# Kernel tuning notes

Measured on AMD Instinct MI355X. Metric: run time of the kernel, lower is better.

## Reference

```python
import jax, jax.numpy as jnp
import numpy as np

D_MODEL = 2048
NUM_EXPERTS = 64
TOP_K = 2
ALPHA = 0.01


def setup_inputs() -> dict:
    key = jax.random.key(0)
    kx, kw = jax.random.split(key)
    x = jax.random.normal(kx, (4, 4096, D_MODEL), dtype=jnp.float32)
    # kaiming-uniform-ish gate weight, bound = 1/sqrt(d_model)
    bound = 1.0 / np.sqrt(D_MODEL)
    W = jax.random.uniform(kw, (NUM_EXPERTS, D_MODEL), dtype=jnp.float32,
                           minval=-bound, maxval=bound)
    return {"x": x, "W": W}


def reference(x, W):
    bsz, seq, h = x.shape
    xf = x.reshape(-1, h)                       # [N, h], N = bsz*seq
    logits = xf @ W.T                            # [N, E]
    scores = jax.nn.softmax(logits, axis=-1)     # [N, E]
    topk_weight, topk_idx = jax.lax.top_k(scores, TOP_K)  # [N, k], [N, k]
    if TOP_K > 1:
        topk_weight = topk_weight / (topk_weight.sum(axis=-1, keepdims=True) + 1e-9)
    # aux loss (training path, alpha > 0)
    one_hot = jax.nn.one_hot(topk_idx.reshape(-1), NUM_EXPERTS, dtype=jnp.float32)
    freq = one_hot.mean(axis=0)                  # [E]
    Pi = scores.mean(axis=0)                     # [E]
    fi = freq * NUM_EXPERTS
    aux_loss = (Pi * fi).sum() * ALPHA
    return topk_weight, topk_idx, aux_loss
```

## Files before the change

### kernel.cpp

```cpp
#include <hip/hip_runtime.h>
#include <math.h>


#define D_MODEL     2048
#define NUM_EXPERTS 64
#define N_ROWS      16384
#define ALPHA       0.01f

#define BR      32
#define BK      32
#define THREADS 256

#define SX 36
#define SW 68
#define SL 72

__global__ __launch_bounds__(THREADS)
void router_fused(const float* __restrict__ x, const float* __restrict__ W,
                  float* __restrict__ out_w, float* __restrict__ out_i,
                  float* __restrict__ g_pi, float* __restrict__ g_cnt) {
    __shared__ float lx[BR * SX];
    __shared__ float lw[BK * SW];
    __shared__ float ll[BR * SL];
    __shared__ float apx[4][NUM_EXPERTS];
    __shared__ float acn[4][NUM_EXPERTS];

    const int tid = threadIdx.x;
    const int rb  = blockIdx.x * BR;

    const int srow = tid >> 3;
    const int skb  = (tid & 7) * 4;

    const float* xg  = x + (size_t)(rb + srow) * D_MODEL + skb;
    const float* wg0 = W + (size_t)srow        * D_MODEL + skb;
    const float* wg1 = W + (size_t)(srow + 32) * D_MODEL + skb;

    const int tx = tid & 15;
    const int ty = tid >> 4;
    const int r0 = ty * 2, r1 = ty * 2 + 1;
    const int eb = tx * 4;

    float acc[2][4] = {{0.f,0.f,0.f,0.f},{0.f,0.f,0.f,0.f}};

    float4 px  = *(const float4*)(xg);
    float4 pw0 = *(const float4*)(wg0);
    float4 pw1 = *(const float4*)(wg1);

    for (int kc = 0; kc < D_MODEL / BK; ++kc) {
        __syncthreads();
        *(float4*)&lx[srow * SX + skb] = px;
        lw[(skb + 0) * SW + srow] = pw0.x;
        lw[(skb + 1) * SW + srow] = pw0.y;
        lw[(skb + 2) * SW + srow] = pw0.z;
        lw[(skb + 3) * SW + srow] = pw0.w;
        lw[(skb + 0) * SW + srow + 32] = pw1.x;
        lw[(skb + 1) * SW + srow + 32] = pw1.y;
        lw[(skb + 2) * SW + srow + 32] = pw1.z;
        lw[(skb + 3) * SW + srow + 32] = pw1.w;
        if (kc + 1 < D_MODEL / BK) {
            const int o = (kc + 1) * BK;
            px  = *(const float4*)(xg  + o);
            pw0 = *(const float4*)(wg0 + o);
            pw1 = *(const float4*)(wg1 + o);
        }
        __syncthreads();

        #pragma unroll
        for (int kk = 0; kk < BK / 4; ++kk) {
            const float4 xa = *(const float4*)&lx[r0 * SX + kk * 4];
            const float4 xb = *(const float4*)&lx[r1 * SX + kk * 4];
            const float4 w0 = *(const float4*)&lw[(kk * 4 + 0) * SW + eb];
            const float4 w1 = *(const float4*)&lw[(kk * 4 + 1) * SW + eb];
            const float4 w2 = *(const float4*)&lw[(kk * 4 + 2) * SW + eb];
            const float4 w3 = *(const float4*)&lw[(kk * 4 + 3) * SW + eb];

            acc[0][0] += xa.x*w0.x + xa.y*w1.x + xa.z*w2.x + xa.w*w3.x;
            acc[0][1] += xa.x*w0.y + xa.y*w1.y + xa.z*w2.y + xa.w*w3.y;
            acc[0][2] += xa.x*w0.z + xa.y*w1.z + xa.z*w2.z + xa.w*w3.z;
            acc[0][3] += xa.x*w0.w + xa.y*w1.w + xa.z*w2.w + xa.w*w3.w;

            acc[1][0] += xb.x*w0.x + xb.y*w1.x + xb.z*w2.x + xb.w*w3.x;
            acc[1][1] += xb.x*w0.y + xb.y*w1.y + xb.z*w2.y + xb.w*w3.y;
            acc[1][2] += xb.x*w0.z + xb.y*w1.z + xb.z*w2.z + xb.w*w3.z;
            acc[1][3] += xb.x*w0.w + xb.y*w1.w + xb.z*w2.w + xb.w*w3.w;
        }
    }

    *(float4*)&ll[r0 * SL + eb] = make_float4(acc[0][0], acc[0][1], acc[0][2], acc[0][3]);
    *(float4*)&ll[r1 * SL + eb] = make_float4(acc[1][0], acc[1][1], acc[1][2], acc[1][3]);
    __syncthreads();

    const int wv   = tid >> 6;
    const int lane = tid & 63;
    float pi_acc  = 0.f;
    float cnt_acc = 0.f;

    for (int r8 = 0; r8 < 8; ++r8) {
        const int row = wv * 8 + r8;
        const float lg = ll[row * SL + lane];

        float m = lg;
        #pragma unroll
        for (int off = 32; off; off >>= 1) m = fmaxf(m, __shfl_xor(m, off));
        const float e = expf(lg - m);
        float s = e;
        #pragma unroll
        for (int off = 32; off; off >>= 1) s += __shfl_xor(s, off);
        const float score = e / s;

        float v1 = score; int i1 = lane;
        #pragma unroll
        for (int off = 32; off; off >>= 1) {
            const float ov = __shfl_xor(v1, off);
            const int   oi = __shfl_xor(i1, off);
            if (ov > v1 || (ov == v1 && oi < i1)) { v1 = ov; i1 = oi; }
        }
        float v2 = (lane == i1) ? -1.f : score; int i2 = lane;
        #pragma unroll
        for (int off = 32; off; off >>= 1) {
            const float ov = __shfl_xor(v2, off);
            const int   oi = __shfl_xor(i2, off);
            if (ov > v2 || (ov == v2 && oi < i2)) { v2 = ov; i2 = oi; }
        }

        if (lane == 0) {
            const int grow = rb + row;
            const float denom = v1 + v2 + 1e-9f;
            out_w[grow * 2 + 0] = v1 / denom;
            out_w[grow * 2 + 1] = v2 / denom;
            out_i[grow * 2 + 0] = (float)i1;
            out_i[grow * 2 + 1] = (float)i2;
        }

        pi_acc  += score;
        cnt_acc += (float)((lane == i1) + (lane == i2));
    }

    apx[wv][lane] = pi_acc;
    acn[wv][lane] = cnt_acc;
    __syncthreads();

    if (tid < NUM_EXPERTS) {
        const float p = apx[0][tid] + apx[1][tid] + apx[2][tid] + apx[3][tid];
        const float c = acn[0][tid] + acn[1][tid] + acn[2][tid] + acn[3][tid];
        atomicAdd(&g_pi[tid],  p);
        atomicAdd(&g_cnt[tid], c);
    }
}

__global__ void router_finalize(const float* __restrict__ g_pi,
                                const float* __restrict__ g_cnt,
                                float* __restrict__ aux_out) {
    const int lane = threadIdx.x;
    const float pi = g_pi[lane] * (1.0f / (float)N_ROWS);
    const float fi = g_cnt[lane] * (64.0f / (float)(N_ROWS * 2));
    float v = pi * fi;
    #pragma unroll
    for (int off = 32; off; off >>= 1) v += __shfl_xor(v, off);
    if (lane == 0) aux_out[0] = v * ALPHA;
}

extern "C" void kernel_launch(void* const* d_in, const int* in_sizes, int n_in,
                              void* d_out, int out_size, void* d_ws, size_t ws_size,
                              hipStream_t stream) {
    const float* x = (const float*)d_in[0];
    const float* W = (const float*)d_in[1];

    float* out   = (float*)d_out;
    float* out_w = out;
    float* out_i = out + N_ROWS * 2;
    float* aux   = out + N_ROWS * 4;

    float* g_pi  = (float*)d_ws;
    float* g_cnt = g_pi + NUM_EXPERTS;

    hipMemsetAsync(d_ws, 0, 2 * NUM_EXPERTS * sizeof(float), stream);

    router_fused<<<dim3(N_ROWS / BR), dim3(THREADS), 0, stream>>>(
        x, W, out_w, out_i, g_pi, g_cnt);
    router_finalize<<<dim3(1), dim3(64), 0, stream>>>(g_pi, g_cnt, aux);
}
```

Measured before the change: 249.3 us.

## Split-K router GEMM with large register tiles and async LDS loads

Replaces the fused per-32-row kernel with a split-K GEMM: 256-row blocks by 8 K-slices, each thread holding an 8x8 register tile, double-buffered LDS filled through global_load_lds with an XOR swizzle. Partial logits go to workspace, and a separate softmax/top-k kernel sums the slices. This targets the low arithmetic intensity and redundant W reloads of the old small tile, which was latency-bound. In exchange it writes and reads 8x16384x64 floats of partials and adds a kernel launch.

```diff
diff --git a/kernel.cpp b/kernel.cpp
--- a/kernel.cpp
+++ b/kernel.cpp
@@ -7,97 +7,129 @@
 #define N_ROWS      16384
 #define ALPHA       0.01f
 
-#define BR      32
-#define BK      32
+#define SLICES  8
+#define KSLICE  (D_MODEL / SLICES)
+#define BK      16
+#define CHUNKS  (KSLICE / BK)
+#define BR      256
 #define THREADS 256
 
-#define SX 36
-#define SW 68
-#define SL 72
-
-__global__ __launch_bounds__(THREADS)
-void router_fused(const float* __restrict__ x, const float* __restrict__ W,
-                  float* __restrict__ out_w, float* __restrict__ out_i,
-                  float* __restrict__ g_pi, float* __restrict__ g_cnt) {
-    __shared__ float lx[BR * SX];
-    __shared__ float lw[BK * SW];
-    __shared__ float ll[BR * SL];
+__global__ __launch_bounds__(THREADS, 2)
+void router_gemm(const float* __restrict__ x, const float* __restrict__ W,
+                 float* __restrict__ partial) {
+    __shared__ float lx[2][BR * BK];
+    __shared__ float lw[2][BK * NUM_EXPERTS];
+
+    const int tid  = threadIdx.x;
+    const int lane = tid & 63;
+    const int wv   = tid >> 6;
+    const int tx   = tid & 7;
+    const int ty   = tid >> 3;
+    const int rb   = blockIdx.x * BR;
+    const int kbase = blockIdx.y * KSLICE;
+    const int sw   = (ty >> 1) & 3;
+
+    float4 a0[8], a1[8];
+    #pragma unroll
+    for (int i = 0; i < 8; ++i) {
+        a0[i] = make_float4(0.f, 0.f, 0.f, 0.f);
+        a1[i] = make_float4(0.f, 0.f, 0.f, 0.f);
+    }
+
+    const int we = lane;
+    const int wq = wv;
+
+    #define STAGE(buf, t)                                                          \
+    {                                                                              \
+        const int k0 = kbase + (t) * BK;                                           \
+        _Pragma("unroll")                                                          \
+        for (int n = 0; n < 4; ++n) {                                              \
+            const int base_slot = (wv * 4 + n) * 64;                               \
+            const int S  = base_slot + lane;                                       \
+            const int R  = S >> 2;                                                 \
+            const int c  = S & 3;                                                  \
+            const int qs = c ^ (((R & 31) >> 1) & 3);                              \
+            const float* gp = x + (size_t)(rb + R) * D_MODEL + k0 + qs * 4;        \
+            __builtin_amdgcn_global_load_lds(                                      \
+                (const __attribute__((address_space(1))) void*)gp,                 \
+                (__attribute__((address_space(3))) void*)&lx[buf][base_slot * 4],  \
+                16, 0, 0);                                                         \
+        }                                                                          \
+        const float4 wval = *(const float4*)(W + (size_t)we * D_MODEL + k0 + wq * 4); \
+        lw[buf][(wq * 4 + 0) * 64 + we] = wval.x;                                  \
+        lw[buf][(wq * 4 + 1) * 64 + we] = wval.y;                                  \
+        lw[buf][(wq * 4 + 2) * 64 + we] = wval.z;                                  \
+        lw[buf][(wq * 4 + 3) * 64 + we] = wval.w;                                  \
+    }
+
+    #define COMPUTE(buf)                                                           \
+    {                                                                              \
+        _Pragma("unroll")                                                          \
+        for (int q = 0; q < 4; ++q) {                                              \
+            float4 xr[8];                                                          \
+            const int cq = (q ^ sw) * 4;                                           \
+            _Pragma("unroll")                                                      \
+            for (int i = 0; i < 8; ++i)                                            \
+                xr[i] = *(const float4*)&lx[buf][(ty + i * 32) * BK + cq];         \
+            _Pragma("unroll")                                                      \
+            for (int j = 0; j < 4; ++j) {                                          \
+                const int k = q * 4 + j;                                           \
+                const float4 wa = *(const float4*)&lw[buf][k * 64 + tx * 4];       \
+                const float4 wb = *(const float4*)&lw[buf][k * 64 + 32 + tx * 4];  \
+                _Pragma("unroll")                                                  \
+                for (int i = 0; i < 8; ++i) {                                      \
+                    const float xv = (j == 0) ? xr[i].x : (j == 1) ? xr[i].y       \
+                                   : (j == 2) ? xr[i].z : xr[i].w;                 \
+                    a0[i].x += xv * wa.x; a0[i].y += xv * wa.y;                    \
+                    a0[i].z += xv * wa.z; a0[i].w += xv * wa.w;                    \
+                    a1[i].x += xv * wb.x; a1[i].y += xv * wb.y;                    \
+                    a1[i].z += xv * wb.z; a1[i].w += xv * wb.w;                    \
+                }                                                                  \
+            }                                                                      \
+        }                                                                          \
+    }
+
+    STAGE(0, 0)
+    int buf = 0;
+    for (int t = 0; t < CHUNKS; ++t) {
+        __syncthreads();
+        if (t + 1 < CHUNKS) STAGE(buf ^ 1, t + 1)
+        COMPUTE(buf)
+        buf ^= 1;
+    }
+
+    const size_t srow = (size_t)blockIdx.y * N_ROWS + rb;
+    #pragma unroll
+    for (int i = 0; i < 8; ++i) {
+        float* p = partial + (srow + ty + i * 32) * NUM_EXPERTS;
+        *(float4*)(p + tx * 4)      = a0[i];
+        *(float4*)(p + 32 + tx * 4) = a1[i];
+    }
+    #undef STAGE
+    #undef COMPUTE
+}
+
+__global__ __launch_bounds__(256)
+void router_softmax(const float* __restrict__ partial,
+                    float* __restrict__ out_w, float* __restrict__ out_i,
+                    float* __restrict__ g_pi, float* __restrict__ g_cnt) {
     __shared__ float apx[4][NUM_EXPERTS];
     __shared__ float acn[4][NUM_EXPERTS];
 
-    const int tid = threadIdx.x;
-    const int rb  = blockIdx.x * BR;
-
-    const int srow = tid >> 3;
-    const int skb  = (tid & 7) * 4;
-
-    const float* xg  = x + (size_t)(rb + srow) * D_MODEL + skb;
-    const float* wg0 = W + (size_t)srow        * D_MODEL + skb;
-    const float* wg1 = W + (size_t)(srow + 32) * D_MODEL + skb;
-
-    const int tx = tid & 15;
-    const int ty = tid >> 4;
-    const int r0 = ty * 2, r1 = ty * 2 + 1;
-    const int eb = tx * 4;
-
-    float acc[2][4] = {{0.f,0.f,0.f,0.f},{0.f,0.f,0.f,0.f}};
-
-    float4 px  = *(const float4*)(xg);
-    float4 pw0 = *(const float4*)(wg0);
-    float4 pw1 = *(const float4*)(wg1);
-
-    for (int kc = 0; kc < D_MODEL / BK; ++kc) {
-        __syncthreads();
-        *(float4*)&lx[srow * SX + skb] = px;
-        lw[(skb + 0) * SW + srow] = pw0.x;
-        lw[(skb + 1) * SW + srow] = pw0.y;
-        lw[(skb + 2) * SW + srow] = pw0.z;
-        lw[(skb + 3) * SW + srow] = pw0.w;
-        lw[(skb + 0) * SW + srow + 32] = pw1.x;
-        lw[(skb + 1) * SW + srow + 32] = pw1.y;
-        lw[(skb + 2) * SW + srow + 32] = pw1.z;
-        lw[(skb + 3) * SW + srow + 32] = pw1.w;
-        if (kc + 1 < D_MODEL / BK) {
-            const int o = (kc + 1) * BK;
-            px  = *(const float4*)(xg  + o);
-            pw0 = *(const float4*)(wg0 + o);
-            pw1 = *(const float4*)(wg1 + o);
-        }
-        __syncthreads();
-
-        #pragma unroll
-        for (int kk = 0; kk < BK / 4; ++kk) {
-            const float4 xa = *(const float4*)&lx[r0 * SX + kk * 4];
-            const float4 xb = *(const float4*)&lx[r1 * SX + kk * 4];
-            const float4 w0 = *(const float4*)&lw[(kk * 4 + 0) * SW + eb];
-            const float4 w1 = *(const float4*)&lw[(kk * 4 + 1) * SW + eb];
-            const float4 w2 = *(const float4*)&lw[(kk * 4 + 2) * SW + eb];
-            const float4 w3 = *(const float4*)&lw[(kk * 4 + 3) * SW + eb];
-
-            acc[0][0] += xa.x*w0.x + xa.y*w1.x + xa.z*w2.x + xa.w*w3.x;
-            acc[0][1] += xa.x*w0.y + xa.y*w1.y + xa.z*w2.y + xa.w*w3.y;
-            acc[0][2] += xa.x*w0.z + xa.y*w1.z + xa.z*w2.z + xa.w*w3.z;
-            acc[0][3] += xa.x*w0.w + xa.y*w1.w + xa.z*w2.w + xa.w*w3.w;
-
-            acc[1][0] += xb.x*w0.x + xb.y*w1.x + xb.z*w2.x + xb.w*w3.x;
-            acc[1][1] += xb.x*w0.y + xb.y*w1.y + xb.z*w2.y + xb.w*w3.y;
-            acc[1][2] += xb.x*w0.z + xb.y*w1.z + xb.z*w2.z + xb.w*w3.z;
-            acc[1][3] += xb.x*w0.w + xb.y*w1.w + xb.z*w2.w + xb.w*w3.w;
-        }
-    }
-
-    *(float4*)&ll[r0 * SL + eb] = make_float4(acc[0][0], acc[0][1], acc[0][2], acc[0][3]);
-    *(float4*)&ll[r1 * SL + eb] = make_float4(acc[1][0], acc[1][1], acc[1][2], acc[1][3]);
-    __syncthreads();
-
+    const int tid  = threadIdx.x;
+    const int lane = tid & 63;
     const int wv   = tid >> 6;
-    const int lane = tid & 63;
-    float pi_acc  = 0.f;
-    float cnt_acc = 0.f;
-
-    for (int r8 = 0; r8 < 8; ++r8) {
-        const int row = wv * 8 + r8;
-        const float lg = ll[row * SL + lane];
+    const int wave_id = blockIdx.x * 4 + wv;
+
+    float pi_acc = 0.f, cnt_acc = 0.f;
+
+    for (int rr = 0; rr < 8; ++rr) {
+        const int row = wave_id * 8 + rr;
+
+        float lg = 0.f;
+        #pragma unroll
+        for (int s = 0; s < SLICES; ++s)
+            lg += partial[((size_t)s * N_ROWS + row) * NUM_EXPERTS + lane];
 
         float m = lg;
         #pragma unroll
@@ -124,12 +156,11 @@
         }
 
         if (lane == 0) {
-            const int grow = rb + row;
             const float denom = v1 + v2 + 1e-9f;
-            out_w[grow * 2 + 0] = v1 / denom;
-            out_w[grow * 2 + 1] = v2 / denom;
-            out_i[grow * 2 + 0] = (float)i1;
-            out_i[grow * 2 + 1] = (float)i2;
+            out_w[row * 2 + 0] = v1 / denom;
+            out_w[row * 2 + 1] = v2 / denom;
+            out_i[row * 2 + 0] = (float)i1;
+            out_i[row * 2 + 1] = (float)i2;
         }
 
         pi_acc  += score;
@@ -171,12 +202,13 @@
     float* out_i = out + N_ROWS * 2;
     float* aux   = out + N_ROWS * 4;
 
-    float* g_pi  = (float*)d_ws;
-    float* g_cnt = g_pi + NUM_EXPERTS;
-
-    hipMemsetAsync(d_ws, 0, 2 * NUM_EXPERTS * sizeof(float), stream);
-
-    router_fused<<<dim3(N_ROWS / BR), dim3(THREADS), 0, stream>>>(
-        x, W, out_w, out_i, g_pi, g_cnt);
+    float* g_pi    = (float*)d_ws;
+    float* g_cnt   = g_pi + NUM_EXPERTS;
+    float* partial = (float*)d_ws + 256;
+
+    hipMemsetAsync(d_ws, 0, 512, stream);
+
+    router_gemm<<<dim3(N_ROWS / BR, SLICES), dim3(THREADS), 0, stream>>>(x, W, partial);
+    router_softmax<<<dim3(N_ROWS / 32), dim3(256), 0, stream>>>(partial, out_w, out_i, g_pi, g_cnt);
     router_finalize<<<dim3(1), dim3(64), 0, stream>>>(g_pi, g_cnt, aux);
 }
```

Result: no change. 248.8 us (-0.2%).

## Use split-fp16 MFMA for router GEMM with prepacked swizzled weight image

Applied to the files above, without the earlier changes.

Replaces the scalar FP32 FMA GEMM with MFMA 16x16x32 f16 instructions. Each fp32 value is split into a scaled hi/lo fp16 pair and three products are accumulated to approximate fp32 precision. A prep kernel packs W into a swizzled chunked layout that is loaded into LDS with global_load_lds and double buffered. Block size grows to 512 threads with BK 64. The aim is to move compute onto the matrix cores and cut LDS traffic. The split-precision trick risks small differences in logits that could flip top-k ties, and it adds an extra prep kernel per call.

```diff
diff --git a/kernel.cpp b/kernel.cpp
--- a/kernel.cpp
+++ b/kernel.cpp
@@ -1,103 +1,143 @@
 #include <hip/hip_runtime.h>
 #include <math.h>
-
-
-#define D_MODEL     2048
-#define NUM_EXPERTS 64
-#define N_ROWS      16384
-#define ALPHA       0.01f
-
+#include <stdint.h>
+
+
+#define D_MODEL 2048
+#define NE      64
+#define N_ROWS  16384
+#define ALPHA   0.01f
 #define BR      32
-#define BK      32
-#define THREADS 256
-
-#define SX 36
-#define SW 68
-#define SL 72
-
-__global__ __launch_bounds__(THREADS)
-void router_fused(const float* __restrict__ x, const float* __restrict__ W,
-                  float* __restrict__ out_w, float* __restrict__ out_i,
-                  float* __restrict__ g_pi, float* __restrict__ g_cnt) {
-    __shared__ float lx[BR * SX];
-    __shared__ float lw[BK * SW];
-    __shared__ float ll[BR * SL];
-    __shared__ float apx[4][NUM_EXPERTS];
-    __shared__ float acn[4][NUM_EXPERTS];
-
-    const int tid = threadIdx.x;
-    const int rb  = blockIdx.x * BR;
-
-    const int srow = tid >> 3;
-    const int skb  = (tid & 7) * 4;
-
-    const float* xg  = x + (size_t)(rb + srow) * D_MODEL + skb;
-    const float* wg0 = W + (size_t)srow        * D_MODEL + skb;
-    const float* wg1 = W + (size_t)(srow + 32) * D_MODEL + skb;
-
-    const int tx = tid & 15;
-    const int ty = tid >> 4;
-    const int r0 = ty * 2, r1 = ty * 2 + 1;
-    const int eb = tx * 4;
-
-    float acc[2][4] = {{0.f,0.f,0.f,0.f},{0.f,0.f,0.f,0.f}};
-
-    float4 px  = *(const float4*)(xg);
-    float4 pw0 = *(const float4*)(wg0);
-    float4 pw1 = *(const float4*)(wg1);
-
-    for (int kc = 0; kc < D_MODEL / BK; ++kc) {
+#define BK      64
+#define NCH     (D_MODEL / BK)
+#define THREADS 512
+
+typedef _Float16 f16x8 __attribute__((ext_vector_type(8)));
+typedef float    f32x4 __attribute__((ext_vector_type(4)));
+
+union U4 { uint32_t u[4]; uint4 v; };
+union F8 { uint32_t u[4]; f16x8 v; };
+
+__device__ __forceinline__ uint32_t pack_hl(float xs) {
+    _Float16 h = (_Float16)xs;
+    float hf = (float)h;
+    _Float16 l = (_Float16)(xs - hf);
+    union { _Float16 f; uint16_t b; } ch, cl;
+    ch.f = h; cl.f = l;
+    return (uint32_t)ch.b | ((uint32_t)cl.b << 16);
+}
+
+#define GLD16(src, dst) __builtin_amdgcn_global_load_lds( \
+    (const __attribute__((address_space(1))) void*)(src), \
+    (__attribute__((address_space(3))) void*)(dst), 16, 0, 0)
+
+__global__ __launch_bounds__(256)
+void w_prep(const float* __restrict__ W, uint32_t* __restrict__ img) {
+    const int idx = blockIdx.x * 256 + threadIdx.x;
+    const int e = idx >> 11, k = idx & 2047;
+    const uint32_t u = pack_hl(W[idx] * 1024.0f);
+    const int c = k >> 6, kl = k & 63, su = kl >> 2, d = kl & 3;
+    img[(size_t)c * 4096 + (e * 16 + (su ^ (e & 7))) * 4 + d] = u;
+}
+
+__global__ __launch_bounds__(THREADS, 4)
+void router_mfma(const float* __restrict__ x, const uint32_t* __restrict__ wimg,
+                 float* __restrict__ out_w, float* __restrict__ out_i,
+                 float* __restrict__ g_pi, float* __restrict__ g_cnt) {
+    __shared__ __align__(16) uint32_t sm[2 * 2048 + 2 * 4096];
+    __shared__ float apx[8][NE], acn[8][NE];
+
+    uint32_t* lx = sm;
+    uint32_t* lw = sm + 4096;
+    float*    ll = (float*)sm;
+
+    const int tid  = threadIdx.x;
+    const int lane = tid & 63;
+    const int wv   = tid >> 6;
+    const int rb   = blockIdx.x * BR;
+
+    const int srow = tid >> 4;
+    const int ssu  = tid & 15;
+    const float* xg = x + (size_t)(rb + srow) * D_MODEL + ssu * 4;
+    const int xw_off = (srow * 16 + (ssu ^ (srow & 7))) * 4;
+
+    const int mt = wv >> 2, nt = wv & 3;
+    const int arow = mt * 16 + (lane & 15);
+    const int be   = nt * 16 + (lane & 15);
+    const int kq   = lane >> 4;
+    const int ap = arow & 7, bp = be & 7;
+
+    f32x4 acc = {0.f, 0.f, 0.f, 0.f};
+
+    {
+        const float4 p0 = *(const float4*)xg;
+        uint4 w0;
+        w0.x = pack_hl(p0.x * 256.f); w0.y = pack_hl(p0.y * 256.f);
+        w0.z = pack_hl(p0.z * 256.f); w0.w = pack_hl(p0.w * 256.f);
+        *(uint4*)(lx + xw_off) = w0;
+        GLD16(wimg + (size_t)tid * 4,         lw + tid * 4);
+        GLD16(wimg + (size_t)(tid + 512) * 4, lw + (tid + 512) * 4);
+    }
+    float4 px = *(const float4*)(xg + BK);
+    __syncthreads();
+
+    for (int t = 0; t < NCH; ++t) {
+        const int buf = t & 1, nbuf = buf ^ 1;
+
+        if (t + 1 < NCH) {
+            const uint32_t* ws = wimg + (size_t)(t + 1) * 4096;
+            GLD16(ws + (size_t)tid * 4,         lw + nbuf * 4096 + tid * 4);
+            GLD16(ws + (size_t)(tid + 512) * 4, lw + nbuf * 4096 + (tid + 512) * 4);
+        }
+
+        const uint32_t* lxb = lx + buf * 2048;
+        const uint32_t* lwb = lw + buf * 4096;
+        #pragma unroll
+        for (int ks = 0; ks < 2; ++ks) {
+            const int su0 = ks * 8 + kq * 2;
+            U4 a0, a1, b0, b1;
+            a0.v = *(const uint4*)(lxb + (arow * 16 + ( su0      ^ ap)) * 4);
+            a1.v = *(const uint4*)(lxb + (arow * 16 + ((su0 + 1) ^ ap)) * 4);
+            b0.v = *(const uint4*)(lwb + (be   * 16 + ( su0      ^ bp)) * 4);
+            b1.v = *(const uint4*)(lwb + (be   * 16 + ((su0 + 1) ^ bp)) * 4);
+            F8 ah, al, bh, bl;
+            #pragma unroll
+            for (int p = 0; p < 2; ++p) {
+                ah.u[p]     = __builtin_amdgcn_perm(a0.u[2*p+1], a0.u[2*p], 0x05040100u);
+                al.u[p]     = __builtin_amdgcn_perm(a0.u[2*p+1], a0.u[2*p], 0x07060302u);
+                ah.u[2 + p] = __builtin_amdgcn_perm(a1.u[2*p+1], a1.u[2*p], 0x05040100u);
+                al.u[2 + p] = __builtin_amdgcn_perm(a1.u[2*p+1], a1.u[2*p], 0x07060302u);
+                bh.u[p]     = __builtin_amdgcn_perm(b0.u[2*p+1], b0.u[2*p], 0x05040100u);
+                bl.u[p]     = __builtin_amdgcn_perm(b0.u[2*p+1], b0.u[2*p], 0x07060302u);
+                bh.u[2 + p] = __builtin_amdgcn_perm(b1.u[2*p+1], b1.u[2*p], 0x05040100u);
+                bl.u[2 + p] = __builtin_amdgcn_perm(b1.u[2*p+1], b1.u[2*p], 0x07060302u);
+            }
+            acc = __builtin_amdgcn_mfma_f32_16x16x32_f16(ah.v, bh.v, acc, 0, 0, 0);
+            acc = __builtin_amdgcn_mfma_f32_16x16x32_f16(ah.v, bl.v, acc, 0, 0, 0);
+            acc = __builtin_amdgcn_mfma_f32_16x16x32_f16(al.v, bh.v, acc, 0, 0, 0);
+        }
+
+        if (t + 1 < NCH) {
+            uint4 wo;
+            wo.x = pack_hl(px.x * 256.f); wo.y = pack_hl(px.y * 256.f);
+            wo.z = pack_hl(px.z * 256.f); wo.w = pack_hl(px.w * 256.f);
+            *(uint4*)(lx + nbuf * 2048 + xw_off) = wo;
+            if (t + 2 < NCH) px = *(const float4*)(xg + (size_t)(t + 2) * BK);
+        }
         __syncthreads();
-        *(float4*)&lx[srow * SX + skb] = px;
-        lw[(skb + 0) * SW + srow] = pw0.x;
-        lw[(skb + 1) * SW + srow] = pw0.y;
-        lw[(skb + 2) * SW + srow] = pw0.z;
-        lw[(skb + 3) * SW + srow] = pw0.w;
-        lw[(skb + 0) * SW + srow + 32] = pw1.x;
-        lw[(skb + 1) * SW + srow + 32] = pw1.y;
-        lw[(skb + 2) * SW + srow + 32] = pw1.z;
-        lw[(skb + 3) * SW + srow + 32] = pw1.w;
-        if (kc + 1 < D_MODEL / BK) {
-            const int o = (kc + 1) * BK;
-            px  = *(const float4*)(xg  + o);
-            pw0 = *(const float4*)(wg0 + o);
-            pw1 = *(const float4*)(wg1 + o);
-        }
-        __syncthreads();
-
-        #pragma unroll
-        for (int kk = 0; kk < BK / 4; ++kk) {
-            const float4 xa = *(const float4*)&lx[r0 * SX + kk * 4];
-            const float4 xb = *(const float4*)&lx[r1 * SX + kk * 4];
-            const float4 w0 = *(const float4*)&lw[(kk * 4 + 0) * SW + eb];
-            const float4 w1 = *(const float4*)&lw[(kk * 4 + 1) * SW + eb];
-            const float4 w2 = *(const float4*)&lw[(kk * 4 + 2) * SW + eb];
-            const float4 w3 = *(const float4*)&lw[(kk * 4 + 3) * SW + eb];
-
-            acc[0][0] += xa.x*w0.x + xa.y*w1.x + xa.z*w2.x + xa.w*w3.x;
-            acc[0][1] += xa.x*w0.y + xa.y*w1.y + xa.z*w2.y + xa.w*w3.y;
-            acc[0][2] += xa.x*w0.z + xa.y*w1.z + xa.z*w2.z + xa.w*w3.z;
-            acc[0][3] += xa.x*w0.w + xa.y*w1.w + xa.z*w2.w + xa.w*w3.w;
-
-            acc[1][0] += xb.x*w0.x + xb.y*w1.x + xb.z*w2.x + xb.w*w3.x;
-            acc[1][1] += xb.x*w0.y + xb.y*w1.y + xb.z*w2.y + xb.w*w3.y;
-            acc[1][2] += xb.x*w0.z + xb.y*w1.z + xb.z*w2.z + xb.w*w3.z;
-            acc[1][3] += xb.x*w0.w + xb.y*w1.w + xb.z*w2.w + xb.w*w3.w;
-        }
-    }
-
-    *(float4*)&ll[r0 * SL + eb] = make_float4(acc[0][0], acc[0][1], acc[0][2], acc[0][3]);
-    *(float4*)&ll[r1 * SL + eb] = make_float4(acc[1][0], acc[1][1], acc[1][2], acc[1][3]);
+    }
+
+    #pragma unroll
+    for (int r = 0; r < 4; ++r) {
+        const int row = mt * 16 + kq * 4 + r;
+        ll[row * 68 + be] = acc[r] * (1.0f / 262144.0f);
+    }
     __syncthreads();
 
-    const int wv   = tid >> 6;
-    const int lane = tid & 63;
-    float pi_acc  = 0.f;
-    float cnt_acc = 0.f;
-
-    for (int r8 = 0; r8 < 8; ++r8) {
-        const int row = wv * 8 + r8;
-        const float lg = ll[row * SL + lane];
+    float pi_acc = 0.f, cnt_acc = 0.f;
+    for (int rr = 0; rr < 4; ++rr) {
+        const int row = wv * 4 + rr;
+        const float lg = ll[row * 68 + lane];
 
         float m = lg;
         #pragma unroll
@@ -131,7 +171,6 @@
             out_i[grow * 2 + 0] = (float)i1;
             out_i[grow * 2 + 1] = (float)i2;
         }
-
         pi_acc  += score;
         cnt_acc += (float)((lane == i1) + (lane == i2));
     }
@@ -140,9 +179,10 @@
     acn[wv][lane] = cnt_acc;
     __syncthreads();
 
-    if (tid < NUM_EXPERTS) {
-        const float p = apx[0][tid] + apx[1][tid] + apx[2][tid] + apx[3][tid];
-        const float c = acn[0][tid] + acn[1][tid] + acn[2][tid] + acn[3][tid];
+    if (tid < NE) {
+        float p = 0.f, c = 0.f;
+        #pragma unroll
+        for (int w = 0; w < 8; ++w) { p += apx[w][tid]; c += acn[w][tid]; }
         atomicAdd(&g_pi[tid],  p);
         atomicAdd(&g_cnt[tid], c);
     }
@@ -171,12 +211,14 @@
     float* out_i = out + N_ROWS * 2;
     float* aux   = out + N_ROWS * 4;
 
-    float* g_pi  = (float*)d_ws;
-    float* g_cnt = g_pi + NUM_EXPERTS;
-
-    hipMemsetAsync(d_ws, 0, 2 * NUM_EXPERTS * sizeof(float), stream);
-
-    router_fused<<<dim3(N_ROWS / BR), dim3(THREADS), 0, stream>>>(
-        x, W, out_w, out_i, g_pi, g_cnt);
+    float*    g_pi  = (float*)d_ws;
+    float*    g_cnt = g_pi + NE;
+    uint32_t* wimg  = (uint32_t*)d_ws + 256;
+
+    hipMemsetAsync(d_ws, 0, 512, stream);
+
+    w_prep<<<dim3(512), dim3(256), 0, stream>>>(W, wimg);
+    router_mfma<<<dim3(N_ROWS / BR), dim3(THREADS), 0, stream>>>(
+        x, wimg, out_w, out_i, g_pi, g_cnt);
     router_finalize<<<dim3(1), dim3(64), 0, stream>>>(g_pi, g_cnt, aux);
 }
```

Result: faster. 218.3 us (-12.4%).
